# Kernel tuning notes

Measured on AMD Instinct MI355X. Metric: run time of the kernel, lower is better.

Reference implementation:

```python
import jax, jax.numpy as jnp
import numpy as np

B, S, D, H = 1, 2048, 1024, 16
HD = D // H  # head_dim = 64
ROPE_BASE = 10000.0


def setup_inputs() -> dict:
    key = jax.random.key(0)
    k1, k2, k3, k4, k5 = jax.random.split(key, 5)
    std = 0.02
    return {
        "hidden_states": jax.random.normal(k1, (B, S, D), dtype=jnp.float32),
        "attention_mask": jnp.ones((B, S), dtype=jnp.int32),
        "position_ids": jnp.broadcast_to(jnp.arange(S, dtype=jnp.int32), (B, S)),
        "wq": jax.random.normal(k2, (D, D), dtype=jnp.float32) * std,
        "wk": jax.random.normal(k3, (D, D), dtype=jnp.float32) * std,
        "wv": jax.random.normal(k4, (D, D), dtype=jnp.float32) * std,
        "wo": jax.random.normal(k5, (D, D), dtype=jnp.float32) * std,
    }


def _rope_cos_sin(position_ids):
    # standard llama freqs: 1/base^(2i/hd), interleaved-pair rotation
    inv_freq = 1.0 / (ROPE_BASE ** (jnp.arange(0, HD, 2, dtype=jnp.float32) / HD))  # [HD/2]
    freqs = position_ids.astype(jnp.float32)[..., None] * inv_freq  # [B,S,HD/2]
    # add head axis for broadcasting: [B,S,1,HD/2]
    return jnp.cos(freqs)[:, :, None, :], jnp.sin(freqs)[:, :, None, :]


def _apply_rope(x, cos, sin):
    # x: [B,S,H,HD]; pairs (x0,x1) rotated as complex (x0+i*x1)*(cos+i*sin)
    x2 = x.reshape(x.shape[:-1] + (HD // 2, 2))
    x0, x1 = x2[..., 0], x2[..., 1]
    out = jnp.stack([x0 * cos - x1 * sin, x0 * sin + x1 * cos], axis=-1)
    return out.reshape(x.shape)


def _attention(hidden_states, attention_mask, position_ids, wq, wk, wv, wo):
    xq = (hidden_states @ wq).reshape(B, S, H, HD)
    xk = (hidden_states @ wk).reshape(B, S, H, HD)
    xv = (hidden_states @ wv).reshape(B, S, H, HD)

    cos, sin = _rope_cos_sin(position_ids)
    xq = _apply_rope(xq, cos, sin)
    xk = _apply_rope(xk, cos, sin)

    # combined causal + padding mask -> additive bias
    causal = jnp.tril(jnp.ones((S, S), dtype=bool))[None, None]  # [1,1,S,S]
    pad = (attention_mask > 0)[:, None, None, :]  # [B,1,1,S]
    mask = jnp.logical_and(causal, pad)
    neg = jnp.finfo(jnp.float32).min
    bias = jnp.where(mask, 0.0, neg).astype(jnp.float32)

    scale = 1.0 / np.sqrt(HD).astype(np.float32)
    scores = jnp.einsum("bqhd,bkhd->bhqk", xq, xk) * scale + bias  # [B,H,S,S]
    attn_weights = jax.nn.softmax(scores, axis=-1)

    attn_output = jnp.einsum("bhqk,bkhd->bqhd", attn_weights, xv)
    attn_output = attn_output.reshape(B, S, D)
    return attn_output @ wo


def reference(hidden_states, attention_mask, position_ids, wq, wk, wv, wo):
    return _attention(hidden_states, attention_mask, position_ids, wq, wk, wv, wo)
```

## Files before the change

kernel.cpp:

```cpp
#include <hip/hip_runtime.h>
#include <stdint.h>

#define SEQ 2048
#define DMODEL 1024
#define NHEAD 16
#define HDIM 64
#define KCH 256
#define NCH 8
#define NIT32 288

typedef unsigned short u16;
typedef __attribute__((ext_vector_type(4))) float f32x4;
typedef __attribute__((ext_vector_type(8))) __bf16 bf16x8;
typedef __attribute__((ext_vector_type(8))) u16 u16x8;

__device__ __forceinline__ u16 f2bf(float f) {
  unsigned int u = __builtin_bit_cast(unsigned int, f);
  unsigned int r = (u + 0x7FFFu + ((u >> 16) & 1u)) >> 16;
  return (u16)r;
}
__device__ __forceinline__ float bf2f(u16 b) {
  unsigned int u = ((unsigned int)b) << 16;
  return __builtin_bit_cast(float, u);
}
__device__ __forceinline__ bf16x8 load8(const u16* p) {
  return __builtin_bit_cast(bf16x8, *(const u16x8*)p);
}
__device__ __forceinline__ void gl_lds16(const void* g, void* l) {
  __builtin_amdgcn_global_load_lds(
      (const __attribute__((address_space(1))) unsigned int*)g,
      (__attribute__((address_space(3))) unsigned int*)l, 16, 0, 0);
}

__global__ __launch_bounds__(256) void convert_x(const float* __restrict__ X,
                                                 u16* __restrict__ Xb) {
  int i = (blockIdx.x * 256 + threadIdx.x) * 4;
  float4 v = *(const float4*)(X + i);
  union { u16 s[4]; uint2 u; } o;
  o.s[0] = f2bf(v.x); o.s[1] = f2bf(v.y); o.s[2] = f2bf(v.z); o.s[3] = f2bf(v.w);
  *(uint2*)(Xb + i) = o.u;
}

__global__ __launch_bounds__(256) void transpose_w(
    const float* __restrict__ W0, const float* __restrict__ W1,
    const float* __restrict__ W2, const float* __restrict__ W3,
    u16* __restrict__ T0, u16* __restrict__ T1,
    u16* __restrict__ T2, u16* __restrict__ T3) {
  __shared__ u16 tile[64][65];
  int bz = blockIdx.z;
  const float* W = bz == 0 ? W0 : bz == 1 ? W1 : bz == 2 ? W2 : W3;
  u16* T = bz == 0 ? T0 : bz == 1 ? T1 : bz == 2 ? T2 : T3;
  int n0 = blockIdx.x * 64, k0 = blockIdx.y * 64;
  int t = threadIdx.x;
#pragma unroll 4
  for (int i = 0; i < 16; ++i) {
    int idx = i * 256 + t;
    int r = idx >> 6, c = idx & 63;
    tile[r][c] = f2bf(W[(k0 + r) * 1024 + n0 + c]);
  }
  __syncthreads();
#pragma unroll 4
  for (int i = 0; i < 16; ++i) {
    int idx = i * 256 + t;
    int r = idx >> 6, c = idx & 63;
    T[(n0 + r) * 1024 + k0 + c] = tile[c][r];
  }
}

template <int BM, int BN, int NMATS, bool OUTF32>
__global__ __launch_bounds__(256) void gemm_bf16(
    const u16* __restrict__ A, const u16* __restrict__ B0,
    const u16* __restrict__ B1, const u16* __restrict__ B2,
    u16* __restrict__ O0, u16* __restrict__ O1, u16* __restrict__ O2,
    float* __restrict__ OF) {
  constexpr int MI = BM / 32, NI = BN / 32;
  constexpr int LA = BM / 64, LB = BN / 64;
  __shared__ u16 As[BM * 32];
  __shared__ u16 Bs[BN * 32];
  const int t = threadIdx.x;
  const int lane = t & 63, w = t >> 6;
  const int g = lane >> 4, li = lane & 15;
  const int n0g = blockIdx.x * BN;
  const int mat = n0g >> 10;
  const int n0 = n0g & 1023;
  const u16* Bp = (NMATS == 1 || mat == 0) ? B0 : (mat == 1 ? B1 : B2);
  const int m0 = blockIdx.y * BM;
  const int wm = (w >> 1) * (BM / 2), wn = (w & 1) * (BN / 2);
  f32x4 acc[MI][NI] = {};
  for (int k0 = 0; k0 < 1024; k0 += 32) {
#pragma unroll
    for (int it = 0; it < LA; ++it) {
      int L = it * 2048 + t * 8;
      int r = L >> 5, c = L & 31;
      gl_lds16(A + (m0 + r) * 1024 + k0 + c, (char*)As + it * 4096 + w * 1024);
    }
#pragma unroll
    for (int it = 0; it < LB; ++it) {
      int L = it * 2048 + t * 8;
      int r = L >> 5, c = L & 31;
      gl_lds16(Bp + (n0 + r) * 1024 + k0 + c, (char*)Bs + it * 4096 + w * 1024);
    }
    __syncthreads();
    bf16x8 af[MI], bfr[NI];
#pragma unroll
    for (int mi = 0; mi < MI; ++mi) af[mi] = load8(&As[(wm + mi * 16 + li) * 32 + g * 8]);
#pragma unroll
    for (int ni = 0; ni < NI; ++ni) bfr[ni] = load8(&Bs[(wn + ni * 16 + li) * 32 + g * 8]);
#pragma unroll
    for (int mi = 0; mi < MI; ++mi)
#pragma unroll
      for (int ni = 0; ni < NI; ++ni)
        acc[mi][ni] = __builtin_amdgcn_mfma_f32_16x16x32_bf16(af[mi], bfr[ni], acc[mi][ni], 0, 0, 0);
    __syncthreads();
  }
  u16* Ob = (NMATS == 1 || mat == 0) ? O0 : (mat == 1 ? O1 : O2);
#pragma unroll
  for (int mi = 0; mi < MI; ++mi)
#pragma unroll
    for (int ni = 0; ni < NI; ++ni)
#pragma unroll
      for (int r = 0; r < 4; ++r) {
        int m = m0 + wm + mi * 16 + g * 4 + r;
        int n = n0 + wn + ni * 16 + li;
        float v = acc[mi][ni][r];
        if (OUTF32) OF[m * 1024 + n] = v;
        else Ob[m * 1024 + n] = f2bf(v);
      }
}

__global__ __launch_bounds__(256) void rope_qk(u16* __restrict__ Qb, u16* __restrict__ Kb,
                                               const int* __restrict__ pos_ids) {
  int gid = blockIdx.x * 256 + threadIdx.x;
  int s = gid >> 9;
  int rem = gid & 511;
  int h = rem >> 5, i = rem & 31;
  float pos = (float)pos_ids[s];
  float inv = exp2f(-(float)i * (13.287712379549449f / 32.0f));
  float ang = pos * inv;
  float sn, cs;
  sincosf(ang, &sn, &cs);
  int base = s * 1024 + h * 64 + 2 * i;
  {
    float x0 = bf2f(Qb[base]), x1 = bf2f(Qb[base + 1]);
    Qb[base]     = f2bf((x0 * cs - x1 * sn) * 0.125f);
    Qb[base + 1] = f2bf((x0 * sn + x1 * cs) * 0.125f);
  }
  {
    float x0 = bf2f(Kb[base]), x1 = bf2f(Kb[base + 1]);
    Kb[base]     = f2bf(x0 * cs - x1 * sn);
    Kb[base + 1] = f2bf(x0 * sn + x1 * cs);
  }
}

__global__ __launch_bounds__(256) void v_transpose(const u16* __restrict__ Vb,
                                                   u16* __restrict__ Vt) {
  __shared__ u16 tile[64][65];
  const int t = threadIdx.x;
  const int s0 = blockIdx.x * 64, h = blockIdx.y;
#pragma unroll 4
  for (int i = 0; i < 16; ++i) {
    int idx = i * 256 + t;
    int r = idx >> 6, c = idx & 63;
    tile[r][c] = Vb[(s0 + r) * 1024 + h * 64 + c];
  }
  __syncthreads();
#pragma unroll 4
  for (int i = 0; i < 16; ++i) {
    int idx = i * 256 + t;
    int d = idx >> 6, sc = idx & 63;
    Vt[h * (64 * 2048) + d * 2048 + s0 + sc] = tile[sc][d];
  }
}

__global__ __launch_bounds__(256) void attn_partial(
    const u16* __restrict__ Qb, const u16* __restrict__ Kb,
    const u16* __restrict__ Vt, const int* __restrict__ amask,
    float* __restrict__ Mpart, float* __restrict__ Lpart, u16* __restrict__ Opart) {
  const int t = threadIdx.x, lane = t & 63, w = t >> 6;
  const int g = lane >> 4, li = lane & 15;
  const int bid = blockIdx.x;
  const int h = bid & 15;
  const int j = (bid >> 4) * 4 + w;
  __shared__ u16 Plds[4][2][16][72];
  const u16* Vh = Vt + h * (64 * 2048);
  const int c = (j >= 280) ? 7 : (j >= 264) ? 6 : (j >= 240) ? 5 : (j >= 208) ? 4
              : (j >= 168) ? 3 : (j >= 120) ? 2 : (j >= 64) ? 1 : 0;
  const int qb = 8 * c + (j - (64 * c - 4 * c * (c - 1)));
  const int q0 = qb * 32;
  const int kstart = c * KCH;
  const int kend = min(kstart + KCH, q0 + 32);
  bf16x8 qf[2][2];
#pragma unroll
  for (int a = 0; a < 2; ++a)
#pragma unroll
    for (int hf = 0; hf < 2; ++hf)
      qf[a][hf] = load8(Qb + (q0 + a * 16 + li) * 1024 + h * 64 + hf * 32 + g * 8);
  f32x4 acc[2][4] = {};
  float mrow[2][4], lrow[2][4];
#pragma unroll
  for (int a = 0; a < 2; ++a)
#pragma unroll
    for (int r = 0; r < 4; ++r) { mrow[a][r] = -1e30f; lrow[a][r] = 0.f; }
  for (int k0 = kstart; k0 < kend; k0 += 64) {
    f32x4 sc[2][4] = {};
#pragma unroll
    for (int s = 0; s < 4; ++s) {
      bf16x8 kf0 = load8(Kb + (k0 + s * 16 + li) * 1024 + h * 64 + 0 + g * 8);
      bf16x8 kf1 = load8(Kb + (k0 + s * 16 + li) * 1024 + h * 64 + 32 + g * 8);
#pragma unroll
      for (int a = 0; a < 2; ++a) {
        sc[a][s] = __builtin_amdgcn_mfma_f32_16x16x32_bf16(qf[a][0], kf0, sc[a][s], 0, 0, 0);
        sc[a][s] = __builtin_amdgcn_mfma_f32_16x16x32_bf16(qf[a][1], kf1, sc[a][s], 0, 0, 0);
      }
    }
    float sv[2][4][4];
    float tmax[2][4];
#pragma unroll
    for (int a = 0; a < 2; ++a)
#pragma unroll
      for (int r = 0; r < 4; ++r) tmax[a][r] = -1e30f;
#pragma unroll
    for (int s = 0; s < 4; ++s) {
      int key = k0 + s * 16 + li;
      bool kok = (amask[key] != 0);
#pragma unroll
      for (int a = 0; a < 2; ++a)
#pragma unroll
        for (int r = 0; r < 4; ++r) {
          int q = q0 + a * 16 + g * 4 + r;
          float v = (kok && key <= q) ? sc[a][s][r] : -1e30f;
          sv[a][s][r] = v;
          tmax[a][r] = fmaxf(tmax[a][r], v);
        }
    }
#pragma unroll
    for (int m = 1; m < 16; m <<= 1)
#pragma unroll
      for (int a = 0; a < 2; ++a)
#pragma unroll
        for (int r = 0; r < 4; ++r)
          tmax[a][r] = fmaxf(tmax[a][r], __shfl_xor(tmax[a][r], m, 64));
    float alpha[2][4];
#pragma unroll
    for (int a = 0; a < 2; ++a)
#pragma unroll
      for (int r = 0; r < 4; ++r) {
        float mn = fmaxf(mrow[a][r], tmax[a][r]);
        alpha[a][r] = __expf(mrow[a][r] - mn);
        mrow[a][r] = mn;
      }
    float ps[2][4] = {};
#pragma unroll
    for (int s = 0; s < 4; ++s)
#pragma unroll
      for (int a = 0; a < 2; ++a)
#pragma unroll
        for (int r = 0; r < 4; ++r) {
          float p = __expf(sv[a][s][r] - mrow[a][r]);
          ps[a][r] += p;
          Plds[w][a][g * 4 + r][s * 16 + li] = f2bf(p);
        }
#pragma unroll
    for (int m = 1; m < 16; m <<= 1)
#pragma unroll
      for (int a = 0; a < 2; ++a)
#pragma unroll
        for (int r = 0; r < 4; ++r) ps[a][r] += __shfl_xor(ps[a][r], m, 64);
#pragma unroll
    for (int a = 0; a < 2; ++a)
#pragma unroll
      for (int r = 0; r < 4; ++r) lrow[a][r] = lrow[a][r] * alpha[a][r] + ps[a][r];
#pragma unroll
    for (int a = 0; a < 2; ++a)
#pragma unroll
      for (int ti = 0; ti < 4; ++ti)
#pragma unroll
        for (int r = 0; r < 4; ++r) acc[a][ti][r] *= alpha[a][r];
    bf16x8 pf[2][2];
#pragma unroll
    for (int a = 0; a < 2; ++a)
#pragma unroll
      for (int ks = 0; ks < 2; ++ks)
        pf[a][ks] = load8(&Plds[w][a][li][ks * 32 + g * 8]);
#pragma unroll
    for (int ti = 0; ti < 4; ++ti) {
      bf16x8 vf0 = load8(Vh + (ti * 16 + li) * 2048 + k0 + 0 + g * 8);
      bf16x8 vf1 = load8(Vh + (ti * 16 + li) * 2048 + k0 + 32 + g * 8);
#pragma unroll
      for (int a = 0; a < 2; ++a) {
        acc[a][ti] = __builtin_amdgcn_mfma_f32_16x16x32_bf16(pf[a][0], vf0, acc[a][ti], 0, 0, 0);
        acc[a][ti] = __builtin_amdgcn_mfma_f32_16x16x32_bf16(pf[a][1], vf1, acc[a][ti], 0, 0, 0);
      }
    }
  }
  const int idx = (h * 64 + qb) * NCH + c;
  if (li == 0) {
#pragma unroll
    for (int a = 0; a < 2; ++a)
#pragma unroll
      for (int r = 0; r < 4; ++r) {
        Mpart[idx * 32 + a * 16 + g * 4 + r] = mrow[a][r];
        Lpart[idx * 32 + a * 16 + g * 4 + r] = lrow[a][r];
      }
  }
#pragma unroll
  for (int a = 0; a < 2; ++a)
#pragma unroll
    for (int ti = 0; ti < 4; ++ti)
#pragma unroll
      for (int r = 0; r < 4; ++r)
        Opart[idx * 2048 + (a * 16 + g * 4 + r) * 64 + ti * 16 + li] = f2bf(acc[a][ti][r]);
}

__global__ __launch_bounds__(256) void attn_combine(
    const float* __restrict__ Mpart, const float* __restrict__ Lpart,
    const u16* __restrict__ Opart, u16* __restrict__ Ab) {
  const int qb = blockIdx.x, h = blockIdx.y;
  const int t = threadIdx.x;
  const int q = t >> 3, dg = t & 7;
  const int nch = qb / 8 + 1;
  const int base = (h * 64 + qb) * NCH;
  float M = -1e30f;
#pragma unroll
  for (int c = 0; c < NCH; ++c)
    if (c < nch) M = fmaxf(M, Mpart[(base + c) * 32 + q]);
  float L = 0.f;
  float o[8] = {};
#pragma unroll
  for (int c = 0; c < NCH; ++c)
    if (c < nch) {
      float e = __expf(Mpart[(base + c) * 32 + q] - M);
      L += e * Lpart[(base + c) * 32 + q];
      uint4 pk = *(const uint4*)(Opart + (base + c) * 2048 + q * 64 + dg * 8);
      const u16* ps = (const u16*)&pk;
#pragma unroll
      for (int jj = 0; jj < 8; ++jj) o[jj] += e * bf2f(ps[jj]);
    }
  float inv = 1.f / L;
  u16* dst = Ab + (qb * 32 + q) * 1024 + h * 64 + dg * 8;
  union { u16 s[8]; uint4 u; } ou;
#pragma unroll
  for (int jj = 0; jj < 8; ++jj) ou.s[jj] = f2bf(o[jj] * inv);
  *(uint4*)dst = ou.u;
}

extern "C" void kernel_launch(void* const* d_in, const int* in_sizes, int n_in,
                              void* d_out, int out_size, void* d_ws, size_t ws_size,
                              hipStream_t stream) {
  const float* X = (const float*)d_in[0];
  const int* amask = (const int*)d_in[1];
  const int* pos = (const int*)d_in[2];
  const float* wq = (const float*)d_in[3];
  const float* wk = (const float*)d_in[4];
  const float* wv = (const float*)d_in[5];
  const float* wo = (const float*)d_in[6];
  float* out = (float*)d_out;
  char* ws = (char*)d_ws;
  u16* Xb  = (u16*)(ws);
  u16* Wtq = (u16*)(ws + (4u  << 20));
  u16* Wtk = (u16*)(ws + (6u  << 20));
  u16* Wtv = (u16*)(ws + (8u  << 20));
  u16* Wto = (u16*)(ws + (10u << 20));
  u16* Qb  = (u16*)(ws + (12u << 20));
  u16* Kb  = (u16*)(ws + (16u << 20));
  u16* Vb  = (u16*)(ws + (20u << 20));
  u16* Vt  = (u16*)(ws + (24u << 20));
  u16* Ab  = (u16*)(ws + (28u << 20));
  float* Mpart = (float*)(ws + (32u << 20));
  float* Lpart = (float*)(ws + (33u << 20));
  u16*   Opart = (u16*)(ws + (34u << 20));

  convert_x<<<2048, 256, 0, stream>>>(X, Xb);
  transpose_w<<<dim3(16, 16, 4), 256, 0, stream>>>(wq, wk, wv, wo, Wtq, Wtk, Wtv, Wto);
  gemm_bf16<64, 128, 3, false><<<dim3(24, 32), 256, 0, stream>>>(Xb, Wtq, Wtk, Wtv, Qb, Kb, Vb, nullptr);
  rope_qk<<<4096, 256, 0, stream>>>(Qb, Kb, pos);
  v_transpose<<<dim3(32, 16), 256, 0, stream>>>(Vb, Vt);
  attn_partial<<<1152, 256, 0, stream>>>(Qb, Kb, Vt, amask, Mpart, Lpart, Opart);
  attn_combine<<<dim3(64, 16), 256, 0, stream>>>(Mpart, Lpart, Opart, Ab);
  gemm_bf16<64, 64, 1, true><<<dim3(16, 32), 256, 0, stream>>>(Ab, Wto, nullptr, nullptr,
                                                               nullptr, nullptr, nullptr, out);
}
```

Baseline: 117.2 us.

## Use larger key chunks, DPP row reductions, exp2 softmax and ballot-based mask

Doubles the attention key chunk size to 512, which halves the number of partial blocks and the combine work. Row max and row sum reductions now use DPP row moves instead of shfl_xor. The log2(e) factor is folded into the Q scaling so the softmax uses exp2f. The padding mask is loaded once per tile via a ballot, and the causal compare is skipped on tiles that lie fully below the diagonal. Fewer, longer blocks may hurt load balance and occupancy, which a launch_bounds occupancy hint of 3 tries to offset.

New measurement: 121.5 us. 1.04x slower.

```diff
diff --git a/kernel.cpp b/kernel.cpp
--- a/kernel.cpp
+++ b/kernel.cpp
@@ -5,9 +5,8 @@
 #define DMODEL 1024
 #define NHEAD 16
 #define HDIM 64
-#define KCH 256
-#define NCH 8
-#define NIT32 288
+#define KCH 512
+#define NCH 4
 
 typedef unsigned short u16;
 typedef __attribute__((ext_vector_type(4))) float f32x4;
@@ -30,6 +29,25 @@
   __builtin_amdgcn_global_load_lds(
       (const __attribute__((address_space(1))) unsigned int*)g,
       (__attribute__((address_space(3))) unsigned int*)l, 16, 0, 0);
+}
+template <int CTRL>
+__device__ __forceinline__ float dpp_mv(float x) {
+  return __builtin_bit_cast(float,
+      __builtin_amdgcn_update_dpp(0, __builtin_bit_cast(int, x), CTRL, 0xF, 0xF, false));
+}
+__device__ __forceinline__ float rowmax16(float v) {
+  v = fmaxf(v, dpp_mv<0x121>(v));
+  v = fmaxf(v, dpp_mv<0x122>(v));
+  v = fmaxf(v, dpp_mv<0x124>(v));
+  v = fmaxf(v, dpp_mv<0x128>(v));
+  return v;
+}
+__device__ __forceinline__ float rowsum16(float v) {
+  v += dpp_mv<0x121>(v);
+  v += dpp_mv<0x122>(v);
+  v += dpp_mv<0x124>(v);
+  v += dpp_mv<0x128>(v);
+  return v;
 }
 
 __global__ __launch_bounds__(256) void convert_x(const float* __restrict__ X,
@@ -140,10 +158,11 @@
   float sn, cs;
   sincosf(ang, &sn, &cs);
   int base = s * 1024 + h * 64 + 2 * i;
+  const float qs = 0.125f * 1.4426950408889634f;
   {
     float x0 = bf2f(Qb[base]), x1 = bf2f(Qb[base + 1]);
-    Qb[base]     = f2bf((x0 * cs - x1 * sn) * 0.125f);
-    Qb[base + 1] = f2bf((x0 * sn + x1 * cs) * 0.125f);
+    Qb[base]     = f2bf((x0 * cs - x1 * sn) * qs);
+    Qb[base + 1] = f2bf((x0 * sn + x1 * cs) * qs);
   }
   {
     float x0 = bf2f(Kb[base]), x1 = bf2f(Kb[base + 1]);
@@ -172,7 +191,7 @@
   }
 }
 
-__global__ __launch_bounds__(256) void attn_partial(
+__global__ __launch_bounds__(256, 3) void attn_partial(
     const u16* __restrict__ Qb, const u16* __restrict__ Kb,
     const u16* __restrict__ Vt, const int* __restrict__ amask,
     float* __restrict__ Mpart, float* __restrict__ Lpart, u16* __restrict__ Opart) {
@@ -183,9 +202,8 @@
   const int j = (bid >> 4) * 4 + w;
   __shared__ u16 Plds[4][2][16][72];
   const u16* Vh = Vt + h * (64 * 2048);
-  const int c = (j >= 280) ? 7 : (j >= 264) ? 6 : (j >= 240) ? 5 : (j >= 208) ? 4
-              : (j >= 168) ? 3 : (j >= 120) ? 2 : (j >= 64) ? 1 : 0;
-  const int qb = 8 * c + (j - (64 * c - 4 * c * (c - 1)));
+  const int c = (j >= 144) ? 3 : (j >= 112) ? 2 : (j >= 64) ? 1 : 0;
+  const int qb = 16 * c + (j - (c == 0 ? 0 : c == 1 ? 64 : c == 2 ? 112 : 144));
   const int q0 = qb * 32;
   const int kstart = c * KCH;
   const int kend = min(kstart + KCH, q0 + 32);
@@ -202,6 +220,8 @@
 #pragma unroll
     for (int r = 0; r < 4; ++r) { mrow[a][r] = -1e30f; lrow[a][r] = 0.f; }
   for (int k0 = kstart; k0 < kend; k0 += 64) {
+    int kidx = k0 + lane;
+    unsigned long long kmsk = __ballot(amask[kidx < SEQ ? kidx : SEQ - 1] != 0);
     f32x4 sc[2][4] = {};
 #pragma unroll
     for (int s = 0; s < 4; ++s) {
@@ -213,69 +233,68 @@
         sc[a][s] = __builtin_amdgcn_mfma_f32_16x16x32_bf16(qf[a][1], kf1, sc[a][s], 0, 0, 0);
       }
     }
-    float sv[2][4][4];
     float tmax[2][4];
 #pragma unroll
     for (int a = 0; a < 2; ++a)
 #pragma unroll
       for (int r = 0; r < 4; ++r) tmax[a][r] = -1e30f;
-#pragma unroll
-    for (int s = 0; s < 4; ++s) {
-      int key = k0 + s * 16 + li;
-      bool kok = (amask[key] != 0);
+    if (k0 + 63 <= q0) {
+#pragma unroll
+      for (int s = 0; s < 4; ++s) {
+        bool kok = ((kmsk >> (s * 16 + li)) & 1ull) != 0;
+#pragma unroll
+        for (int a = 0; a < 2; ++a)
+#pragma unroll
+          for (int r = 0; r < 4; ++r) {
+            float v = kok ? sc[a][s][r] : -1e30f;
+            sc[a][s][r] = v;
+            tmax[a][r] = fmaxf(tmax[a][r], v);
+          }
+      }
+    } else {
+#pragma unroll
+      for (int s = 0; s < 4; ++s) {
+        int key = k0 + s * 16 + li;
+        bool kok = ((kmsk >> (s * 16 + li)) & 1ull) != 0;
+#pragma unroll
+        for (int a = 0; a < 2; ++a)
+#pragma unroll
+          for (int r = 0; r < 4; ++r) {
+            int q = q0 + a * 16 + g * 4 + r;
+            float v = (kok && key <= q) ? sc[a][s][r] : -1e30f;
+            sc[a][s][r] = v;
+            tmax[a][r] = fmaxf(tmax[a][r], v);
+          }
+      }
+    }
+    float alpha[2][4];
+#pragma unroll
+    for (int a = 0; a < 2; ++a)
+#pragma unroll
+      for (int r = 0; r < 4; ++r) {
+        float mn = fmaxf(mrow[a][r], rowmax16(tmax[a][r]));
+        alpha[a][r] = exp2f(mrow[a][r] - mn);
+        mrow[a][r] = mn;
+      }
+    float ps[2][4] = {};
+#pragma unroll
+    for (int s = 0; s < 4; ++s)
 #pragma unroll
       for (int a = 0; a < 2; ++a)
 #pragma unroll
         for (int r = 0; r < 4; ++r) {
-          int q = q0 + a * 16 + g * 4 + r;
-          float v = (kok && key <= q) ? sc[a][s][r] : -1e30f;
-          sv[a][s][r] = v;
-          tmax[a][r] = fmaxf(tmax[a][r], v);
-        }
-    }
-#pragma unroll
-    for (int m = 1; m < 16; m <<= 1)
-#pragma unroll
-      for (int a = 0; a < 2; ++a)
-#pragma unroll
-        for (int r = 0; r < 4; ++r)
-          tmax[a][r] = fmaxf(tmax[a][r], __shfl_xor(tmax[a][r], m, 64));
-    float alpha[2][4];
-#pragma unroll
-    for (int a = 0; a < 2; ++a)
-#pragma unroll
-      for (int r = 0; r < 4; ++r) {
-        float mn = fmaxf(mrow[a][r], tmax[a][r]);
-        alpha[a][r] = __expf(mrow[a][r] - mn);
-        mrow[a][r] = mn;
-      }
-    float ps[2][4] = {};
-#pragma unroll
-    for (int s = 0; s < 4; ++s)
-#pragma unroll
-      for (int a = 0; a < 2; ++a)
-#pragma unroll
-        for (int r = 0; r < 4; ++r) {
-          float p = __expf(sv[a][s][r] - mrow[a][r]);
+          float p = exp2f(sc[a][s][r] - mrow[a][r]);
           ps[a][r] += p;
           Plds[w][a][g * 4 + r][s * 16 + li] = f2bf(p);
         }
 #pragma unroll
-    for (int m = 1; m < 16; m <<= 1)
-#pragma unroll
-      for (int a = 0; a < 2; ++a)
-#pragma unroll
-        for (int r = 0; r < 4; ++r) ps[a][r] += __shfl_xor(ps[a][r], m, 64);
-#pragma unroll
     for (int a = 0; a < 2; ++a)
 #pragma unroll
-      for (int r = 0; r < 4; ++r) lrow[a][r] = lrow[a][r] * alpha[a][r] + ps[a][r];
-#pragma unroll
-    for (int a = 0; a < 2; ++a)
-#pragma unroll
-      for (int ti = 0; ti < 4; ++ti)
-#pragma unroll
-        for (int r = 0; r < 4; ++r) acc[a][ti][r] *= alpha[a][r];
+      for (int r = 0; r < 4; ++r) {
+        lrow[a][r] = lrow[a][r] * alpha[a][r] + rowsum16(ps[a][r]);
+#pragma unroll
+        for (int ti = 0; ti < 4; ++ti) acc[a][ti][r] *= alpha[a][r];
+      }
     bf16x8 pf[2][2];
 #pragma unroll
     for (int a = 0; a < 2; ++a)
@@ -318,7 +337,7 @@
   const int qb = blockIdx.x, h = blockIdx.y;
   const int t = threadIdx.x;
   const int q = t >> 3, dg = t & 7;
-  const int nch = qb / 8 + 1;
+  const int nch = qb / 16 + 1;
   const int base = (h * 64 + qb) * NCH;
   float M = -1e30f;
 #pragma unroll
@@ -329,7 +348,7 @@
 #pragma unroll
   for (int c = 0; c < NCH; ++c)
     if (c < nch) {
-      float e = __expf(Mpart[(base + c) * 32 + q] - M);
+      float e = exp2f(Mpart[(base + c) * 32 + q] - M);
       L += e * Lpart[(base + c) * 32 + q];
       uint4 pk = *(const uint4*)(Opart + (base + c) * 2048 + q * 64 + dg * 8);
       const u16* ps = (const u16*)&pk;
@@ -367,15 +386,15 @@
   u16* Vt  = (u16*)(ws + (24u << 20));
   u16* Ab  = (u16*)(ws + (28u << 20));
   float* Mpart = (float*)(ws + (32u << 20));
-  float* Lpart = (float*)(ws + (33u << 20));
-  u16*   Opart = (u16*)(ws + (34u << 20));
+  float* Lpart = (float*)(ws + (34u << 20));
+  u16*   Opart = (u16*)(ws + (36u << 20));
 
   convert_x<<<2048, 256, 0, stream>>>(X, Xb);
   transpose_w<<<dim3(16, 16, 4), 256, 0, stream>>>(wq, wk, wv, wo, Wtq, Wtk, Wtv, Wto);
   gemm_bf16<64, 128, 3, false><<<dim3(24, 32), 256, 0, stream>>>(Xb, Wtq, Wtk, Wtv, Qb, Kb, Vb, nullptr);
   rope_qk<<<4096, 256, 0, stream>>>(Qb, Kb, pos);
   v_transpose<<<dim3(32, 16), 256, 0, stream>>>(Vb, Vt);
-  attn_partial<<<1152, 256, 0, stream>>>(Qb, Kb, Vt, amask, Mpart, Lpart, Opart);
+  attn_partial<<<640, 256, 0, stream>>>(Qb, Kb, Vt, amask, Mpart, Lpart, Opart);
   attn_combine<<<dim3(64, 16), 256, 0, stream>>>(Mpart, Lpart, Opart, Ab);
   gemm_bf16<64, 64, 1, true><<<dim3(16, 32), 256, 0, stream>>>(Ab, Wto, nullptr, nullptr,
                                                                nullptr, nullptr, nullptr, out);
```
